# Performance work log

Measured on AMD Instinct MI355X. Metric: run time of the kernel, lower is better.

## Reference

```python
import jax, jax.numpy as jnp
import numpy as np

BETA = 0.25


def _l2_normalize(v, eps=1e-12):
    # matches torch F.normalize(dim=-1): v / max(||v||, eps)
    n = jnp.linalg.norm(v, axis=-1, keepdims=True)
    return v / jnp.maximum(n, eps)


def _cosine_sim(a, b, eps=1e-8):
    # matches torch F.cosine_similarity(dim=-1)
    na = jnp.maximum(jnp.linalg.norm(a, axis=-1), eps)
    nb = jnp.maximum(jnp.linalg.norm(b, axis=-1), eps)
    return jnp.sum(a * b, axis=-1) / (na * nb)


def setup_inputs() -> dict:
    key = jax.random.key(0)
    k1, k2 = jax.random.split(key)
    B, D, N = 32768, 256, 8192
    x = jax.random.normal(k1, (B, D), dtype=jnp.float32)
    # embedding init: uniform(-1/n_e, 1/n_e) as in the torch module
    embedding = jax.random.uniform(k2, (N, D), dtype=jnp.float32,
                                   minval=-1.0 / N, maxval=1.0 / N)
    return {"x": x, "embedding": embedding}


def reference(x, embedding):
    latent = x                                   # (B, D)
    codebook = embedding                         # (N, D)
    latent_norm = _l2_normalize(latent)
    codebook_norm = _l2_normalize(codebook)
    sim = jnp.einsum('bd,nd->bn', latent_norm, codebook_norm)  # (B, N)
    distances = 1.0 - sim
    indices = jnp.argmin(distances, axis=-1)     # (B,) int
    codebook_vec = codebook[indices]             # (B, D) gather
    dot = jnp.sum(latent * codebook_vec, axis=-1, keepdims=True)
    norm_sq = jnp.sum(codebook_vec * codebook_vec, axis=-1, keepdims=True)
    scalar = dot / (norm_sq + 1e-8)              # (B, 1)
    proj_vec = scalar * codebook_vec             # (B, D)
    # use_ema=True branch: only commitment loss (proj_vec detached)
    commit = _cosine_sim(jax.lax.stop_gradient(proj_vec), latent)
    loss = BETA * jnp.mean(1.0 - commit)
    # straight-through
    x_q = x + jax.lax.stop_gradient(proj_vec - x)
    return (x_q, loss, indices, scalar[:, 0])
```

## Files before the change

### kernel.cpp

```cpp
#include <hip/hip_runtime.h>
#include <hip/hip_bf16.h>
#include <hip/hip_fp16.h>
#include <cstdint>
#include <cstddef>

#define B_ROWS 32768
#define DIM    256
#define NBLK64 128
#define CERT_M 3.0e-3f
#define PRE_M  3.0e-3f

typedef _Float16 f16x8 __attribute__((ext_vector_type(8)));
typedef float    f32x4 __attribute__((ext_vector_type(4)));
typedef unsigned short u16x8 __attribute__((ext_vector_type(8)));

#define WS_XBF     ((size_t)0)
#define WS_CBBF    ((size_t)16777216)
#define WS_TOPINFO ((size_t)20971520)
#define WS_CNORM   ((size_t)54525952)
#define WS_LPART   ((size_t)54591488)

#define OUT_XQ   ((size_t)0)
#define OUT_LOSS ((size_t)8388608)
#define OUT_IDX  ((size_t)8388609)
#define OUT_SCAL ((size_t)(8388609 + 32768))

__device__ inline double wave_sum_d(double v){ for (int d = 1; d < 64; d <<= 1) v += __shfl_xor(v, d); return v; }
__device__ inline unsigned umax_(unsigned a, unsigned b){ return a > b ? a : b; }
__device__ inline unsigned umin_(unsigned a, unsigned b){ return a < b ? a : b; }

__device__ inline float kinvb(unsigned k){ return __uint_as_float(k & 0xFFFFE000u); }

__device__ inline void load16_lds(const void* g, void* l) {
    __builtin_amdgcn_global_load_lds(
        (const __attribute__((address_space(1))) unsigned int*)g,
        (__attribute__((address_space(3))) unsigned int*)l, 16, 0, 0);
}

__global__ __launch_bounds__(256)
void prep_kernel(const float* __restrict__ x, const float* __restrict__ cb,
                 ushort* __restrict__ xbf, ushort* __restrict__ cbbf,
                 double* __restrict__ inv_cnorm) {
    int gw   = blockIdx.x * 4 + (threadIdx.x >> 6);
    int lane = threadIdx.x & 63;
    bool is_cb = gw >= B_ROWS;
    int row  = is_cb ? gw - B_ROWS : gw;
    const float* src = is_cb ? cb + (size_t)row * DIM : x + (size_t)row * DIM;
    ushort*      dst = is_cb ? cbbf + (size_t)row * DIM : xbf + (size_t)row * DIM;

    float4 v = ((const float4*)src)[lane];
    double ss = (double)v.x * v.x + (double)v.y * v.y + (double)v.z * v.z + (double)v.w * v.w;
    ss = wave_sum_d(ss);
    float inv = 1.f / fmaxf(sqrtf((float)ss), 1e-12f);
    ushort4 o;
    o.x = __half_as_ushort(__float2half(v.x * inv));
    o.y = __half_as_ushort(__float2half(v.y * inv));
    o.z = __half_as_ushort(__float2half(v.z * inv));
    o.w = __half_as_ushort(__float2half(v.w * inv));
    ((ushort4*)dst)[lane] = o;
    if (is_cb && lane == 0) inv_cnorm[row] = 1.0 / sqrt(ss);
}

__global__ __launch_bounds__(512, 2)
void simmax_kernel(const ushort* __restrict__ xbf, const ushort* __restrict__ cbbf,
                   uint2* __restrict__ topinfo) {
    __shared__ __align__(16) ushort Cs[2][256 * 64];
    __shared__ __align__(16) ushort Xs[2][256 * 64];

    const int t    = threadIdx.x;
    const int xcd  = blockIdx.x & 7;
    const int lidx = blockIdx.x >> 3;
    const int bm   = xcd * 4 + (lidx & 3);
    const int bn   = lidx >> 2;
    const int cn0  = bm * 256;
    const int rm0  = bn * 256;

    const int wid  = t >> 6, lane = t & 63;
    const int wm   = wid >> 2;
    const int wn   = wid & 3;
    const int q    = lane >> 4, r16 = lane & 15;

    const int srow = t >> 3;
    const int cpos = t & 7;
    const int csrc = cpos ^ (srow & 7);
    const ushort* cbsrc = cbbf + (size_t)(cn0 + srow) * DIM + csrc * 8;
    const ushort* xsrc  = xbf  + (size_t)(rm0 + srow) * DIM + csrc * 8;
    const int ldst = srow * 64 + cpos * 8;

    const int g0  = q ^ (r16 & 7);
    const int g1  = g0 ^ 4;
    const int crb = (wm * 128 + r16) * 64;
    const int xrb = (wn * 64  + r16) * 64;

    f32x4 acc[8][4];
#pragma unroll
    for (int i = 0; i < 8; ++i)
#pragma unroll
        for (int j = 0; j < 4; ++j) acc[i][j] = (f32x4){2.f, 2.f, 2.f, 2.f};

    f16x8 cf[4][2], xf0[2][2], xf1[2][2];

#define SCHED0 __builtin_amdgcn_sched_barrier(0)
#define SBAR do { SCHED0; __builtin_amdgcn_s_barrier(); SCHED0; } while (0)
#define WLG0 do { asm volatile("s_waitcnt lgkmcnt(0)" ::: "memory"); SCHED0; } while (0)
#define WVM(N) do { asm volatile("s_waitcnt vmcnt(" #N ")" ::: "memory"); SCHED0; } while (0)

#define ST_C(B,KT,H) do { \
    load16_lds(cbsrc + ((H)*128     ) * DIM + (KT)*64, &Cs[B][ldst + ((H)*128     ) * 64]); \
    load16_lds(cbsrc + ((H)*128 + 64) * DIM + (KT)*64, &Cs[B][ldst + ((H)*128 + 64) * 64]); \
} while (0)
#define ST_X(B,KT,H) do { \
    load16_lds(xsrc  + ((H)*128     ) * DIM + (KT)*64, &Xs[B][ldst + ((H)*128     ) * 64]); \
    load16_lds(xsrc  + ((H)*128 + 64) * DIM + (KT)*64, &Xs[B][ldst + ((H)*128 + 64) * 64]); \
} while (0)

#define RD_C(HM,B) do { \
    _Pragma("unroll") \
    for (int m2_ = 0; m2_ < 4; ++m2_) { \
        const ushort* p_ = &Cs[B][crb + ((HM)*64 + m2_*16) * 64]; \
        cf[m2_][0] = *(const f16x8*)(p_ + g0 * 8); \
        cf[m2_][1] = *(const f16x8*)(p_ + g1 * 8); \
    } } while (0)
#define RD_X(DST,HN,B) do { \
    _Pragma("unroll") \
    for (int n2_ = 0; n2_ < 2; ++n2_) { \
        const ushort* p_ = &Xs[B][xrb + ((HN)*32 + n2_*16) * 64]; \
        DST[n2_][0] = *(const f16x8*)(p_ + g0 * 8); \
        DST[n2_][1] = *(const f16x8*)(p_ + g1 * 8); \
    } } while (0)

#define MMQ(HM,HN,XF) do { \
    __builtin_amdgcn_s_setprio(1); \
    _Pragma("unroll") \
    for (int m2_ = 0; m2_ < 4; ++m2_) \
    _Pragma("unroll") \
    for (int n2_ = 0; n2_ < 2; ++n2_) \
    _Pragma("unroll") \
    for (int kk_ = 0; kk_ < 2; ++kk_) \
        acc[(HM)*4 + m2_][(HN)*2 + n2_] = __builtin_amdgcn_mfma_f32_16x16x32_f16( \
            cf[m2_][kk_], XF[n2_][kk_], acc[(HM)*4 + m2_][(HN)*2 + n2_], 0, 0, 0); \
    __builtin_amdgcn_s_setprio(0); \
} while (0)

    ST_X(0,0,0); ST_X(0,0,1); ST_C(0,0,0); ST_C(0,0,1);
    ST_X(1,1,0);
    WVM(2); SBAR;

    RD_C(0,0); RD_X(xf0,0,0); ST_X(1,1,1); SBAR; WLG0; MMQ(0,0,xf0); SBAR;
    RD_X(xf1,1,0);            ST_C(1,1,0); SBAR; WLG0; MMQ(0,1,xf1); SBAR;
    RD_C(1,0);                ST_C(1,1,1); SBAR; WLG0; MMQ(1,1,xf1); SBAR;
    ST_X(0,2,0); WVM(2);                   SBAR;       MMQ(1,0,xf0); SBAR;
    RD_C(0,1); RD_X(xf0,0,1); ST_X(0,2,1); SBAR; WLG0; MMQ(0,0,xf0); SBAR;
    RD_X(xf1,1,1);            ST_C(0,2,0); SBAR; WLG0; MMQ(0,1,xf1); SBAR;
    RD_C(1,1);                ST_C(0,2,1); SBAR; WLG0; MMQ(1,1,xf1); SBAR;
    ST_X(1,3,0); WVM(2);                   SBAR;       MMQ(1,0,xf0); SBAR;
    RD_C(0,0); RD_X(xf0,0,0); ST_X(1,3,1); SBAR; WLG0; MMQ(0,0,xf0); SBAR;
    RD_X(xf1,1,0);            ST_C(1,3,0); SBAR; WLG0; MMQ(0,1,xf1); SBAR;
    RD_C(1,0);                ST_C(1,3,1); SBAR; WLG0; MMQ(1,1,xf1); SBAR;
    WVM(0);                                SBAR;       MMQ(1,0,xf0); SBAR;
    RD_C(0,1); RD_X(xf0,0,1);              SBAR; WLG0; MMQ(0,0,xf0); SBAR;
    RD_X(xf1,1,1);                         SBAR; WLG0; MMQ(0,1,xf1); SBAR;
    RD_C(1,1);                             SBAR; WLG0; MMQ(1,1,xf1); SBAR;
                                                       MMQ(1,0,xf0);

    const int cb0 = 8191 - (cn0 + wm * 128 + q * 4);
#pragma unroll
    for (int ni = 0; ni < 4; ++ni) {
        unsigned r1v[2], r2v[2];
#pragma unroll
        for (int b2 = 0; b2 < 2; ++b2) {
            const unsigned cbb = (unsigned)(cb0 - b2 * 64);
            unsigned k[16];
#pragma unroll
            for (int m2 = 0; m2 < 4; ++m2)
#pragma unroll
                for (int r = 0; r < 4; ++r)
                    k[m2 * 4 + r] = (__float_as_uint(acc[b2 * 4 + m2][ni][r]) & 0xFFFFE000u)
                                  | (cbb - (unsigned)(m2 * 16 + r));
            unsigned h0[8], l0[8];
#pragma unroll
            for (int i = 0; i < 8; ++i) { h0[i] = umax_(k[2*i], k[2*i+1]); l0[i] = umin_(k[2*i], k[2*i+1]); }
            unsigned h1[4], l1[4];
#pragma unroll
            for (int i = 0; i < 4; ++i) { h1[i] = umax_(h0[2*i], h0[2*i+1]); l1[i] = umin_(h0[2*i], h0[2*i+1]); }
            unsigned h2a = umax_(h1[0], h1[1]), l2a = umin_(h1[0], h1[1]);
            unsigned h2b = umax_(h1[2], h1[3]), l2b = umin_(h1[2], h1[3]);
            unsigned m1  = umax_(h2a, h2b);
            unsigned lt  = umin_(h2a, h2b);
            unsigned s0  = umax_(umax_(umax_(l0[0], l0[1]), umax_(l0[2], l0[3])),
                                 umax_(umax_(l0[4], l0[5]), umax_(l0[6], l0[7])));
            unsigned s1  = umax_(umax_(l1[0], l1[1]), umax_(l1[2], l1[3]));
            unsigned m2v = umax_(umax_(s0, s1), umax_(umax_(l2a, l2b), lt));
#pragma unroll
            for (int d = 16; d < 64; d <<= 1) {
                unsigned o1 = (unsigned)__shfl_xor((int)m1, d);
                unsigned o2 = (unsigned)__shfl_xor((int)m2v, d);
                unsigned lo = m1 < o1 ? m1 : o1;
                m2v = umax_(umax_(m2v, o2), lo);
                m1  = umax_(m1, o1);
            }
            r1v[b2] = m1; r2v[b2] = m2v;
        }
        if (q == 0) {
            const int rowg = rm0 + wn * 64 + ni * 16 + r16;
            uint4 o; o.x = r1v[0]; o.y = r2v[0]; o.z = r1v[1]; o.w = r2v[1];
            *(uint4*)(topinfo + (size_t)rowg * NBLK64 + bm * 4 + wm * 2) = o;
        }
    }
#undef SCHED0
#undef SBAR
#undef WLG0
#undef WVM
#undef ST_C
#undef ST_X
#undef RD_C
#undef RD_X
#undef MMQ
}

__global__ __launch_bounds__(256)
void argmax_kernel(const float* __restrict__ x, const float* __restrict__ cb,
                   const ushort* __restrict__ xbf, const ushort* __restrict__ cbbf,
                   const uint2* __restrict__ topinfo,
                   const double* __restrict__ inv_cnorm,
                   float* __restrict__ out, float* __restrict__ loss_part) {
    __shared__ float lsum[4];
    const int w    = threadIdx.x >> 6;
    const int row  = blockIdx.x * 4 + w;
    const int lane = threadIdx.x & 63;

    uint4 tt = ((const uint4*)(topinfo + (size_t)row * NBLK64))[lane];
    unsigned k1[2] = {tt.x, tt.z};
    unsigned k2[2] = {tt.y, tt.w};

    unsigned W = umax_(k1[0], k1[1]);
    for (int d = 1; d < 64; d <<= 1) W = umax_(W, (unsigned)__shfl_xor((int)W, d));
    unsigned R = umax_((k1[0] == W) ? k2[0] : k1[0], (k1[1] == W) ? k2[1] : k1[1]);
    for (int d = 1; d < 64; d <<= 1) R = umax_(R, (unsigned)__shfl_xor((int)R, d));

    float v1w = kinvb(W);
    float rvf = kinvb(R);

    float4 xv = ((const float4*)(x + (size_t)row * DIM))[lane];

    int best_i;
    if (v1w - rvf > CERT_M) {
        best_i = 8191 - (int)(W & 0x1FFFu);
    } else {
        const int c = lane >> 3, e = lane & 7;
        float xh[32];
#pragma unroll
        for (int k4 = 0; k4 < 4; ++k4) {
            u16x8 hx = ((const u16x8*)(xbf + (size_t)row * DIM + e * 32))[k4];
#pragma unroll
            for (int j = 0; j < 8; ++j)
                xh[k4 * 8 + j] = __half2float(__ushort_as_half((ushort)hx[j]));
        }

        double best_s = -1e300;
        int bi = 0x7fffffff;
        auto exact_eval = [&](int n) {
            float4 cv = ((const float4*)(cb + (size_t)n * DIM))[lane];
            double s = (double)xv.x * cv.x + (double)xv.y * cv.y +
                       (double)xv.z * cv.z + (double)xv.w * cv.w;
            s = wave_sum_d(s);
            s *= inv_cnorm[n];
            if (s > best_s || (s == best_s && n < bi)) { best_s = s; bi = n; }
        };

        const float thrblk = v1w - CERT_M;
        const float thrpre = v1w - 2.0f - PRE_M;
        float v1f[2] = {kinvb(k1[0]), kinvb(k1[1])};
#pragma unroll
        for (int s = 0; s < 2; ++s) {
            unsigned long long bm = __ballot(v1f[s] >= thrblk);
            while (bm) {
                int src = __ffsll((unsigned long long)bm) - 1;
                bm &= bm - 1;
                int blk = src * 2 + s;
#pragma unroll 1
                for (int sub = 0; sub < 8; ++sub) {
                    int n = blk * 64 + sub * 8 + c;
                    float s0 = 0.f, s1 = 0.f, s2 = 0.f, s3 = 0.f;
#pragma unroll
                    for (int k4 = 0; k4 < 4; ++k4) {
                        u16x8 chv = ((const u16x8*)(cbbf + (size_t)n * DIM + e * 32))[k4];
#pragma unroll
                        for (int j = 0; j < 8; ++j) {
                            float cf = __half2float(__ushort_as_half((ushort)chv[j]));
                            float xf = xh[k4 * 8 + j];
                            if ((j & 3) == 0) s0 = fmaf(xf, cf, s0);
                            else if ((j & 3) == 1) s1 = fmaf(xf, cf, s1);
                            else if ((j & 3) == 2) s2 = fmaf(xf, cf, s2);
                            else s3 = fmaf(xf, cf, s3);
                        }
                    }
                    float ps = (s0 + s1) + (s2 + s3);
                    ps += __shfl_xor(ps, 1);
                    ps += __shfl_xor(ps, 2);
                    ps += __shfl_xor(ps, 4);
                    unsigned long long sv = __ballot(e == 0 && ps >= thrpre);
                    while (sv) {
                        int b = __ffsll((unsigned long long)sv) - 1;
                        sv &= sv - 1;
                        exact_eval(blk * 64 + sub * 8 + (b >> 3));
                    }
                }
            }
        }
        for (int d = 1; d < 64; d <<= 1) {
            double os = __shfl_xor(best_s, d);
            int    oi = __shfl_xor(bi, d);
            if (os > best_s || (os == best_s && oi < bi)) { best_s = os; bi = oi; }
        }
        best_i = bi;
    }

    float4 cv = ((const float4*)(cb + (size_t)best_i * DIM))[lane];
    float dot = xv.x * cv.x + xv.y * cv.y + xv.z * cv.z + xv.w * cv.w;
    float nsq = cv.x * cv.x + cv.y * cv.y + cv.z * cv.z + cv.w * cv.w;
    float xsq = xv.x * xv.x + xv.y * xv.y + xv.z * xv.z + xv.w * xv.w;
    for (int d = 1; d < 64; d <<= 1) {
        dot += __shfl_xor(dot, d);
        nsq += __shfl_xor(nsq, d);
        xsq += __shfl_xor(xsq, d);
    }
    float scalar = dot / (nsq + 1e-8f);
    float4 pj = {scalar * cv.x, scalar * cv.y, scalar * cv.z, scalar * cv.w};
    ((float4*)(out + OUT_XQ + (size_t)row * DIM))[lane] = pj;

    float pn = fmaxf(sqrtf(scalar * scalar * nsq), 1e-8f);
    float xn = fmaxf(sqrtf(xsq), 1e-8f);
    float commit = (scalar * dot) / (pn * xn);
    if (lane == 0) {
        lsum[w] = 1.f - commit;
        out[OUT_IDX + row]  = (float)best_i;
        out[OUT_SCAL + row] = scalar;
    }
    __syncthreads();
    if (threadIdx.x == 0)
        loss_part[blockIdx.x] = lsum[0] + lsum[1] + lsum[2] + lsum[3];
}

__global__ __launch_bounds__(256)
void loss_kernel(const float* __restrict__ part, float* __restrict__ out) {
    __shared__ float ws_[4];
    float s = 0.f;
    for (int i = threadIdx.x; i < 8192; i += 256) s += part[i];
    for (int d = 1; d < 64; d <<= 1) s += __shfl_xor(s, d);
    if ((threadIdx.x & 63) == 0) ws_[threadIdx.x >> 6] = s;
    __syncthreads();
    if (threadIdx.x == 0)
        out[OUT_LOSS] = 0.25f * (ws_[0] + ws_[1] + ws_[2] + ws_[3]) * (1.0f / 32768.0f);
}

extern "C" void kernel_launch(void* const* d_in, const int* in_sizes, int n_in,
                              void* d_out, int out_size, void* d_ws, size_t ws_size,
                              hipStream_t stream) {
    const float* x  = (const float*)d_in[0];
    const float* cb = (const float*)d_in[1];
    float* out = (float*)d_out;
    char*  ws  = (char*)d_ws;
    ushort* xbf     = (ushort*)(ws + WS_XBF);
    ushort* cbbf    = (ushort*)(ws + WS_CBBF);
    uint2*  topinfo = (uint2*)(ws + WS_TOPINFO);
    double* inv_cn  = (double*)(ws + WS_CNORM);
    float*  loss_part = (float*)(ws + WS_LPART);

    hipLaunchKernelGGL(prep_kernel, dim3((B_ROWS + 8192) / 4), dim3(256), 0, stream,
                       x, cb, xbf, cbbf, inv_cn);
    hipLaunchKernelGGL(simmax_kernel, dim3((B_ROWS / 256) * (8192 / 256)), dim3(512), 0, stream,
                       xbf, cbbf, topinfo);
    hipLaunchKernelGGL(argmax_kernel, dim3(B_ROWS / 4), dim3(256), 0, stream,
                       x, cb, xbf, cbbf, topinfo, inv_cn, out, loss_part);
    hipLaunchKernelGGL(loss_kernel, dim3(1), dim3(256), 0, stream, loss_part, out);
}
```

Before: 334.3 us.

## Make simmax kernel persistent, looping over 16 row tiles with cross-tile prefetch

The similarity/top-2 kernel becomes persistent: 256 blocks each handle one codebook tile and iterate over 16 row tiles of x. Loads for the next tile's first K-slices are issued during the tail of the current tile, so launch/prologue cost is amortized and the pipeline stays full across tiles. The codebook tile stays in the same block, but the codebook tile is reloaded every iteration anyway; the risk is lower parallelism (256 blocks with 2 per CU may underfill 256 CUs) and a serial epilogue reduction that is now not overlapped with other blocks' MMA.

```diff
diff --git a/kernel.cpp b/kernel.cpp
--- a/kernel.cpp
+++ b/kernel.cpp
@@ -67,24 +67,22 @@
     __shared__ __align__(16) ushort Cs[2][256 * 64];
     __shared__ __align__(16) ushort Xs[2][256 * 64];
 
-    const int t    = threadIdx.x;
-    const int xcd  = blockIdx.x & 7;
-    const int lidx = blockIdx.x >> 3;
-    const int bm   = xcd * 4 + (lidx & 3);
-    const int bn   = lidx >> 2;
+    const int t512 = threadIdx.x;
+    const int b    = blockIdx.x;
+    const int bm   = (b & 7) * 4 + ((b >> 3) & 3);
+    const int bn0  = (b >> 5) * 16;
     const int cn0  = bm * 256;
-    const int rm0  = bn * 256;
-
-    const int wid  = t >> 6, lane = t & 63;
+
+    const int wid  = t512 >> 6, lane = t512 & 63;
     const int wm   = wid >> 2;
     const int wn   = wid & 3;
     const int q    = lane >> 4, r16 = lane & 15;
 
-    const int srow = t >> 3;
-    const int cpos = t & 7;
+    const int srow = t512 >> 3;
+    const int cpos = t512 & 7;
     const int csrc = cpos ^ (srow & 7);
-    const ushort* cbsrc = cbbf + (size_t)(cn0 + srow) * DIM + csrc * 8;
-    const ushort* xsrc  = xbf  + (size_t)(rm0 + srow) * DIM + csrc * 8;
+    const ushort* cbsrc  = cbbf + (size_t)(cn0 + srow) * DIM + csrc * 8;
+    const ushort* xfirst = xbf  + ((size_t)bn0 * 256 + srow) * DIM + csrc * 8;
     const int ldst = srow * 64 + cpos * 8;
 
     const int g0  = q ^ (r16 & 7);
@@ -93,11 +91,6 @@
     const int xrb = (wn * 64  + r16) * 64;
 
     f32x4 acc[8][4];
-#pragma unroll
-    for (int i = 0; i < 8; ++i)
-#pragma unroll
-        for (int j = 0; j < 4; ++j) acc[i][j] = (f32x4){2.f, 2.f, 2.f, 2.f};
-
     f16x8 cf[4][2], xf0[2][2], xf1[2][2];
 
 #define SCHED0 __builtin_amdgcn_sched_barrier(0)
@@ -109,9 +102,9 @@
     load16_lds(cbsrc + ((H)*128     ) * DIM + (KT)*64, &Cs[B][ldst + ((H)*128     ) * 64]); \
     load16_lds(cbsrc + ((H)*128 + 64) * DIM + (KT)*64, &Cs[B][ldst + ((H)*128 + 64) * 64]); \
 } while (0)
-#define ST_X(B,KT,H) do { \
-    load16_lds(xsrc  + ((H)*128     ) * DIM + (KT)*64, &Xs[B][ldst + ((H)*128     ) * 64]); \
-    load16_lds(xsrc  + ((H)*128 + 64) * DIM + (KT)*64, &Xs[B][ldst + ((H)*128 + 64) * 64]); \
+#define ST_X(B,KT,H,P) do { \
+    load16_lds((P)  + ((H)*128     ) * DIM + (KT)*64, &Xs[B][ldst + ((H)*128     ) * 64]); \
+    load16_lds((P)  + ((H)*128 + 64) * DIM + (KT)*64, &Xs[B][ldst + ((H)*128 + 64) * 64]); \
 } while (0)
 
 #define RD_C(HM,B) do { \
@@ -142,71 +135,93 @@
     __builtin_amdgcn_s_setprio(0); \
 } while (0)
 
-    ST_X(0,0,0); ST_X(0,0,1); ST_C(0,0,0); ST_C(0,0,1);
-    ST_X(1,1,0);
+#pragma unroll
+    for (int i = 0; i < 8; ++i)
+#pragma unroll
+        for (int j = 0; j < 4; ++j) acc[i][j] = (f32x4){2.f, 2.f, 2.f, 2.f};
+
+    const ushort* xA = xfirst;
+    ST_X(0,0,0,xA); ST_X(0,0,1,xA); ST_C(0,0,0); ST_C(0,0,1);
+    ST_X(1,1,0,xA);
     WVM(2); SBAR;
 
-    RD_C(0,0); RD_X(xf0,0,0); ST_X(1,1,1); SBAR; WLG0; MMQ(0,0,xf0); SBAR;
-    RD_X(xf1,1,0);            ST_C(1,1,0); SBAR; WLG0; MMQ(0,1,xf1); SBAR;
-    RD_C(1,0);                ST_C(1,1,1); SBAR; WLG0; MMQ(1,1,xf1); SBAR;
-    ST_X(0,2,0); WVM(2);                   SBAR;       MMQ(1,0,xf0); SBAR;
-    RD_C(0,1); RD_X(xf0,0,1); ST_X(0,2,1); SBAR; WLG0; MMQ(0,0,xf0); SBAR;
-    RD_X(xf1,1,1);            ST_C(0,2,0); SBAR; WLG0; MMQ(0,1,xf1); SBAR;
-    RD_C(1,1);                ST_C(0,2,1); SBAR; WLG0; MMQ(1,1,xf1); SBAR;
-    ST_X(1,3,0); WVM(2);                   SBAR;       MMQ(1,0,xf0); SBAR;
-    RD_C(0,0); RD_X(xf0,0,0); ST_X(1,3,1); SBAR; WLG0; MMQ(0,0,xf0); SBAR;
-    RD_X(xf1,1,0);            ST_C(1,3,0); SBAR; WLG0; MMQ(0,1,xf1); SBAR;
-    RD_C(1,0);                ST_C(1,3,1); SBAR; WLG0; MMQ(1,1,xf1); SBAR;
-    WVM(0);                                SBAR;       MMQ(1,0,xf0); SBAR;
-    RD_C(0,1); RD_X(xf0,0,1);              SBAR; WLG0; MMQ(0,0,xf0); SBAR;
-    RD_X(xf1,1,1);                         SBAR; WLG0; MMQ(0,1,xf1); SBAR;
-    RD_C(1,1);                             SBAR; WLG0; MMQ(1,1,xf1); SBAR;
-                                                       MMQ(1,0,xf0);
-
-    const int cb0 = 8191 - (cn0 + wm * 128 + q * 4);
-#pragma unroll
-    for (int ni = 0; ni < 4; ++ni) {
-        unsigned r1v[2], r2v[2];
-#pragma unroll
-        for (int b2 = 0; b2 < 2; ++b2) {
-            const unsigned cbb = (unsigned)(cb0 - b2 * 64);
-            unsigned k[16];
-#pragma unroll
-            for (int m2 = 0; m2 < 4; ++m2)
-#pragma unroll
-                for (int r = 0; r < 4; ++r)
-                    k[m2 * 4 + r] = (__float_as_uint(acc[b2 * 4 + m2][ni][r]) & 0xFFFFE000u)
-                                  | (cbb - (unsigned)(m2 * 16 + r));
-            unsigned h0[8], l0[8];
-#pragma unroll
-            for (int i = 0; i < 8; ++i) { h0[i] = umax_(k[2*i], k[2*i+1]); l0[i] = umin_(k[2*i], k[2*i+1]); }
-            unsigned h1[4], l1[4];
-#pragma unroll
-            for (int i = 0; i < 4; ++i) { h1[i] = umax_(h0[2*i], h0[2*i+1]); l1[i] = umin_(h0[2*i], h0[2*i+1]); }
-            unsigned h2a = umax_(h1[0], h1[1]), l2a = umin_(h1[0], h1[1]);
-            unsigned h2b = umax_(h1[2], h1[3]), l2b = umin_(h1[2], h1[3]);
-            unsigned m1  = umax_(h2a, h2b);
-            unsigned lt  = umin_(h2a, h2b);
-            unsigned s0  = umax_(umax_(umax_(l0[0], l0[1]), umax_(l0[2], l0[3])),
-                                 umax_(umax_(l0[4], l0[5]), umax_(l0[6], l0[7])));
-            unsigned s1  = umax_(umax_(l1[0], l1[1]), umax_(l1[2], l1[3]));
-            unsigned m2v = umax_(umax_(s0, s1), umax_(umax_(l2a, l2b), lt));
-#pragma unroll
-            for (int d = 16; d < 64; d <<= 1) {
-                unsigned o1 = (unsigned)__shfl_xor((int)m1, d);
-                unsigned o2 = (unsigned)__shfl_xor((int)m2v, d);
-                unsigned lo = m1 < o1 ? m1 : o1;
-                m2v = umax_(umax_(m2v, o2), lo);
-                m1  = umax_(m1, o1);
+#pragma unroll 1
+    for (int t = 0; t < 16; ++t) {
+        const ushort* xB = (t == 15) ? xfirst : (xA + 256 * DIM);
+
+        RD_C(0,0); RD_X(xf0,0,0); ST_X(1,1,1,xA); SBAR; WLG0; MMQ(0,0,xf0); SBAR;
+        RD_X(xf1,1,0);            ST_C(1,1,0);    SBAR; WLG0; MMQ(0,1,xf1); SBAR;
+        RD_C(1,0);                ST_C(1,1,1);    SBAR; WLG0; MMQ(1,1,xf1); SBAR;
+        ST_X(0,2,0,xA); WVM(2);                   SBAR;       MMQ(1,0,xf0); SBAR;
+        RD_C(0,1); RD_X(xf0,0,1); ST_X(0,2,1,xA); SBAR; WLG0; MMQ(0,0,xf0); SBAR;
+        RD_X(xf1,1,1);            ST_C(0,2,0);    SBAR; WLG0; MMQ(0,1,xf1); SBAR;
+        RD_C(1,1);                ST_C(0,2,1);    SBAR; WLG0; MMQ(1,1,xf1); SBAR;
+        ST_X(1,3,0,xA); WVM(2);                   SBAR;       MMQ(1,0,xf0); SBAR;
+        RD_C(0,0); RD_X(xf0,0,0); ST_X(1,3,1,xA); SBAR; WLG0; MMQ(0,0,xf0); SBAR;
+        RD_X(xf1,1,0);            ST_C(1,3,0);    SBAR; WLG0; MMQ(0,1,xf1); SBAR;
+        RD_C(1,0);                ST_C(1,3,1);    SBAR; WLG0; MMQ(1,1,xf1); SBAR;
+        ST_X(0,0,0,xB); WVM(2);                   SBAR;       MMQ(1,0,xf0); SBAR;
+        RD_C(0,1); RD_X(xf0,0,1); ST_X(0,0,1,xB); SBAR; WLG0; MMQ(0,0,xf0); SBAR;
+        RD_X(xf1,1,1);            ST_C(0,0,0);    SBAR; WLG0; MMQ(0,1,xf1); SBAR;
+        RD_C(1,1);                ST_C(0,0,1);    SBAR; WLG0; MMQ(1,1,xf1); SBAR;
+        ST_X(1,1,0,xB); WVM(2);                   SBAR;       MMQ(1,0,xf0); SBAR;
+
+        const int rm0 = (bn0 + t) * 256;
+        const int cb0 = 8191 - (cn0 + wm * 128 + q * 4);
+#pragma unroll
+        for (int ni = 0; ni < 4; ++ni) {
+            unsigned r1v[2], r2v[2];
+#pragma unroll
+            for (int b2 = 0; b2 < 2; ++b2) {
+                const unsigned cbb = (unsigned)(cb0 - b2 * 64);
+                unsigned k[16];
+#pragma unroll
+                for (int m2 = 0; m2 < 4; ++m2)
+#pragma unroll
+                    for (int r = 0; r < 4; ++r)
+                        k[m2 * 4 + r] = (__float_as_uint(acc[b2 * 4 + m2][ni][r]) & 0xFFFFE000u)
+                                      | (cbb - (unsigned)(m2 * 16 + r));
+                unsigned h0[8], l0[8];
+#pragma unroll
+                for (int i = 0; i < 8; ++i) { h0[i] = umax_(k[2*i], k[2*i+1]); l0[i] = umin_(k[2*i], k[2*i+1]); }
+                unsigned h1[4], l1[4];
+#pragma unroll
+                for (int i = 0; i < 4; ++i) { h1[i] = umax_(h0[2*i], h0[2*i+1]); l1[i] = umin_(h0[2*i], h0[2*i+1]); }
+                unsigned h2a = umax_(h1[0], h1[1]), l2a = umin_(h1[0], h1[1]);
+                unsigned h2b = umax_(h1[2], h1[3]), l2b = umin_(h1[2], h1[3]);
+                unsigned m1  = umax_(h2a, h2b);
+                unsigned lt  = umin_(h2a, h2b);
+                unsigned s0  = umax_(umax_(umax_(l0[0], l0[1]), umax_(l0[2], l0[3])),
+                                     umax_(umax_(l0[4], l0[5]), umax_(l0[6], l0[7])));
+                unsigned s1  = umax_(umax_(l1[0], l1[1]), umax_(l1[2], l1[3]));
+                unsigned m2v = umax_(umax_(s0, s1), umax_(umax_(l2a, l2b), lt));
+#pragma unroll
+                for (int d = 16; d < 64; d <<= 1) {
+                    unsigned o1 = (unsigned)__shfl_xor((int)m1, d);
+                    unsigned o2 = (unsigned)__shfl_xor((int)m2v, d);
+                    unsigned lo = m1 < o1 ? m1 : o1;
+                    m2v = umax_(umax_(m2v, o2), lo);
+                    m1  = umax_(m1, o1);
+                }
+                r1v[b2] = m1; r2v[b2] = m2v;
             }
-            r1v[b2] = m1; r2v[b2] = m2v;
+            if (q == 0) {
+                const int rowg = rm0 + wn * 64 + ni * 16 + r16;
+                uint4 o; o.x = r1v[0]; o.y = r2v[0]; o.z = r1v[1]; o.w = r2v[1];
+                *(uint4*)(topinfo + (size_t)rowg * NBLK64 + bm * 4 + wm * 2) = o;
+            }
         }
-        if (q == 0) {
-            const int rowg = rm0 + wn * 64 + ni * 16 + r16;
-            uint4 o; o.x = r1v[0]; o.y = r2v[0]; o.z = r1v[1]; o.w = r2v[1];
-            *(uint4*)(topinfo + (size_t)rowg * NBLK64 + bm * 4 + wm * 2) = o;
-        }
+
+#pragma unroll
+        for (int i = 0; i < 8; ++i)
+#pragma unroll
+            for (int j = 0; j < 4; ++j) acc[i][j] = (f32x4){2.f, 2.f, 2.f, 2.f};
+
+        xA = xB;
     }
+
+    WVM(0);
+
 #undef SCHED0
 #undef SBAR
 #undef WLG0
@@ -369,7 +384,7 @@
 
     hipLaunchKernelGGL(prep_kernel, dim3((B_ROWS + 8192) / 4), dim3(256), 0, stream,
                        x, cb, xbf, cbbf, inv_cn);
-    hipLaunchKernelGGL(simmax_kernel, dim3((B_ROWS / 256) * (8192 / 256)), dim3(512), 0, stream,
+    hipLaunchKernelGGL(simmax_kernel, dim3(256), dim3(512), 0, stream,
                        xbf, cbbf, topinfo);
     hipLaunchKernelGGL(argmax_kernel, dim3(B_ROWS / 4), dim3(256), 0, stream,
                        x, cb, xbf, cbbf, topinfo, inv_cn, out, loss_part);
```

Result: slower. 428.2 us (+28.1%).

## Restructure simmax K-loop with triple-buffered X tiles and fewer barriers

Applied to the files above, without the earlier changes.

Rewrites the simmax GEMM main loop as a 4-step K loop. X tiles are triple-buffered and codebook fragments are double-buffered in registers (cfA/cfB), so LDS reads for the next half overlap MFMAs. Per-quarter barriers and explicit lgkmcnt waits are dropped in favour of one or two barriers per K step. The top-2 reduction for the first codebook half is interleaved with the last MFMAs to hide its latency. In exchange, LDS use rises from 128 KB to 160 KB per block, which may conflict with the 2-blocks-per-CU launch bound, and register pressure grows.

```diff
diff --git a/kernel.cpp b/kernel.cpp
--- a/kernel.cpp
+++ b/kernel.cpp
@@ -65,7 +65,7 @@
 void simmax_kernel(const ushort* __restrict__ xbf, const ushort* __restrict__ cbbf,
                    uint2* __restrict__ topinfo) {
     __shared__ __align__(16) ushort Cs[2][256 * 64];
-    __shared__ __align__(16) ushort Xs[2][256 * 64];
+    __shared__ __align__(16) ushort Xs[3][256 * 64];
 
     const int t    = threadIdx.x;
     const int xcd  = blockIdx.x & 7;
@@ -89,8 +89,6 @@
 
     const int g0  = q ^ (r16 & 7);
     const int g1  = g0 ^ 4;
-    const int crb = (wm * 128 + r16) * 64;
-    const int xrb = (wn * 64  + r16) * 64;
 
     f32x4 acc[8][4];
 #pragma unroll
@@ -98,38 +96,35 @@
 #pragma unroll
         for (int j = 0; j < 4; ++j) acc[i][j] = (f32x4){2.f, 2.f, 2.f, 2.f};
 
-    f16x8 cf[4][2], xf0[2][2], xf1[2][2];
+    f16x8 cfA[4][2], cfB[4][2], xp[2][2], xq[2][2];
 
 #define SCHED0 __builtin_amdgcn_sched_barrier(0)
-#define SBAR do { SCHED0; __builtin_amdgcn_s_barrier(); SCHED0; } while (0)
-#define WLG0 do { asm volatile("s_waitcnt lgkmcnt(0)" ::: "memory"); SCHED0; } while (0)
+#define SBAR do { __builtin_amdgcn_s_barrier(); SCHED0; } while (0)
 #define WVM(N) do { asm volatile("s_waitcnt vmcnt(" #N ")" ::: "memory"); SCHED0; } while (0)
 
-#define ST_C(B,KT,H) do { \
-    load16_lds(cbsrc + ((H)*128     ) * DIM + (KT)*64, &Cs[B][ldst + ((H)*128     ) * 64]); \
-    load16_lds(cbsrc + ((H)*128 + 64) * DIM + (KT)*64, &Cs[B][ldst + ((H)*128 + 64) * 64]); \
+#define ST4(DST, SRC, KT) do { \
+    load16_lds((SRC) + (size_t)  0 * DIM + (KT)*64, &(DST)[ldst +   0 * 64]); \
+    load16_lds((SRC) + (size_t) 64 * DIM + (KT)*64, &(DST)[ldst +  64 * 64]); \
+    load16_lds((SRC) + (size_t)128 * DIM + (KT)*64, &(DST)[ldst + 128 * 64]); \
+    load16_lds((SRC) + (size_t)192 * DIM + (KT)*64, &(DST)[ldst + 192 * 64]); \
 } while (0)
-#define ST_X(B,KT,H) do { \
-    load16_lds(xsrc  + ((H)*128     ) * DIM + (KT)*64, &Xs[B][ldst + ((H)*128     ) * 64]); \
-    load16_lds(xsrc  + ((H)*128 + 64) * DIM + (KT)*64, &Xs[B][ldst + ((H)*128 + 64) * 64]); \
-} while (0)
-
-#define RD_C(HM,B) do { \
+
+#define RD_C8(DST, BUF, HOFF) do { \
     _Pragma("unroll") \
     for (int m2_ = 0; m2_ < 4; ++m2_) { \
-        const ushort* p_ = &Cs[B][crb + ((HM)*64 + m2_*16) * 64]; \
-        cf[m2_][0] = *(const f16x8*)(p_ + g0 * 8); \
-        cf[m2_][1] = *(const f16x8*)(p_ + g1 * 8); \
+        const ushort* p_ = &(BUF)[(wm * 128 + (HOFF) + m2_ * 16 + r16) * 64]; \
+        DST[m2_][0] = *(const f16x8*)(p_ + g0 * 8); \
+        DST[m2_][1] = *(const f16x8*)(p_ + g1 * 8); \
     } } while (0)
-#define RD_X(DST,HN,B) do { \
+#define RD_X4(DST, BUF, HOFF) do { \
     _Pragma("unroll") \
     for (int n2_ = 0; n2_ < 2; ++n2_) { \
-        const ushort* p_ = &Xs[B][xrb + ((HN)*32 + n2_*16) * 64]; \
+        const ushort* p_ = &(BUF)[(wn * 64 + (HOFF) + n2_ * 16 + r16) * 64]; \
         DST[n2_][0] = *(const f16x8*)(p_ + g0 * 8); \
         DST[n2_][1] = *(const f16x8*)(p_ + g1 * 8); \
     } } while (0)
 
-#define MMQ(HM,HN,XF) do { \
+#define MMQ(CF, XF, HM, HN) do { \
     __builtin_amdgcn_s_setprio(1); \
     _Pragma("unroll") \
     for (int m2_ = 0; m2_ < 4; ++m2_) \
@@ -138,84 +133,96 @@
     _Pragma("unroll") \
     for (int kk_ = 0; kk_ < 2; ++kk_) \
         acc[(HM)*4 + m2_][(HN)*2 + n2_] = __builtin_amdgcn_mfma_f32_16x16x32_f16( \
-            cf[m2_][kk_], XF[n2_][kk_], acc[(HM)*4 + m2_][(HN)*2 + n2_], 0, 0, 0); \
+            CF[m2_][kk_], XF[n2_][kk_], acc[(HM)*4 + m2_][(HN)*2 + n2_], 0, 0, 0); \
     __builtin_amdgcn_s_setprio(0); \
 } while (0)
 
-    ST_X(0,0,0); ST_X(0,0,1); ST_C(0,0,0); ST_C(0,0,1);
-    ST_X(1,1,0);
-    WVM(2); SBAR;
-
-    RD_C(0,0); RD_X(xf0,0,0); ST_X(1,1,1); SBAR; WLG0; MMQ(0,0,xf0); SBAR;
-    RD_X(xf1,1,0);            ST_C(1,1,0); SBAR; WLG0; MMQ(0,1,xf1); SBAR;
-    RD_C(1,0);                ST_C(1,1,1); SBAR; WLG0; MMQ(1,1,xf1); SBAR;
-    ST_X(0,2,0); WVM(2);                   SBAR;       MMQ(1,0,xf0); SBAR;
-    RD_C(0,1); RD_X(xf0,0,1); ST_X(0,2,1); SBAR; WLG0; MMQ(0,0,xf0); SBAR;
-    RD_X(xf1,1,1);            ST_C(0,2,0); SBAR; WLG0; MMQ(0,1,xf1); SBAR;
-    RD_C(1,1);                ST_C(0,2,1); SBAR; WLG0; MMQ(1,1,xf1); SBAR;
-    ST_X(1,3,0); WVM(2);                   SBAR;       MMQ(1,0,xf0); SBAR;
-    RD_C(0,0); RD_X(xf0,0,0); ST_X(1,3,1); SBAR; WLG0; MMQ(0,0,xf0); SBAR;
-    RD_X(xf1,1,0);            ST_C(1,3,0); SBAR; WLG0; MMQ(0,1,xf1); SBAR;
-    RD_C(1,0);                ST_C(1,3,1); SBAR; WLG0; MMQ(1,1,xf1); SBAR;
-    WVM(0);                                SBAR;       MMQ(1,0,xf0); SBAR;
-    RD_C(0,1); RD_X(xf0,0,1);              SBAR; WLG0; MMQ(0,0,xf0); SBAR;
-    RD_X(xf1,1,1);                         SBAR; WLG0; MMQ(0,1,xf1); SBAR;
-    RD_C(1,1);                             SBAR; WLG0; MMQ(1,1,xf1); SBAR;
-                                                       MMQ(1,0,xf0);
+#define TOP2(B2, NI, M1O, M2O) do { \
+    const unsigned cbb_ = (unsigned)(cb0 - (B2) * 64); \
+    unsigned k_[16]; \
+    _Pragma("unroll") \
+    for (int m2_ = 0; m2_ < 4; ++m2_) \
+    _Pragma("unroll") \
+    for (int r_ = 0; r_ < 4; ++r_) \
+        k_[m2_*4+r_] = (__float_as_uint(acc[(B2)*4 + m2_][NI][r_]) & 0xFFFFE000u) \
+                     | (cbb_ - (unsigned)(m2_*16 + r_)); \
+    unsigned h0_[8], l0_[8]; \
+    _Pragma("unroll") \
+    for (int i_ = 0; i_ < 8; ++i_) { h0_[i_] = umax_(k_[2*i_], k_[2*i_+1]); l0_[i_] = umin_(k_[2*i_], k_[2*i_+1]); } \
+    unsigned h1_[4], l1_[4]; \
+    _Pragma("unroll") \
+    for (int i_ = 0; i_ < 4; ++i_) { h1_[i_] = umax_(h0_[2*i_], h0_[2*i_+1]); l1_[i_] = umin_(h0_[2*i_], h0_[2*i_+1]); } \
+    unsigned h2a_ = umax_(h1_[0], h1_[1]), l2a_ = umin_(h1_[0], h1_[1]); \
+    unsigned h2b_ = umax_(h1_[2], h1_[3]), l2b_ = umin_(h1_[2], h1_[3]); \
+    unsigned m1_  = umax_(h2a_, h2b_); \
+    unsigned lt_  = umin_(h2a_, h2b_); \
+    unsigned s0_  = umax_(umax_(umax_(l0_[0], l0_[1]), umax_(l0_[2], l0_[3])), \
+                          umax_(umax_(l0_[4], l0_[5]), umax_(l0_[6], l0_[7]))); \
+    unsigned s1_  = umax_(umax_(l1_[0], l1_[1]), umax_(l1_[2], l1_[3])); \
+    unsigned m2v_ = umax_(umax_(s0_, s1_), umax_(umax_(l2a_, l2b_), lt_)); \
+    _Pragma("unroll") \
+    for (int d_ = 16; d_ < 64; d_ <<= 1) { \
+        unsigned o1_ = (unsigned)__shfl_xor((int)m1_, d_); \
+        unsigned o2_ = (unsigned)__shfl_xor((int)m2v_, d_); \
+        unsigned lo_ = m1_ < o1_ ? m1_ : o1_; \
+        m2v_ = umax_(umax_(m2v_, o2_), lo_); \
+        m1_  = umax_(m1_, o1_); \
+    } \
+    M1O = m1_; M2O = m2v_; \
+} while (0)
+
+    ST4(Cs[0], cbsrc, 0);
+    ST4(Xs[0], xsrc , 0);
+    ST4(Xs[1], xsrc , 1);
+    WVM(4);
+    SBAR;
+    RD_C8(cfA, Cs[0], 0);
 
     const int cb0 = 8191 - (cn0 + wm * 128 + q * 4);
+    unsigned r1a[4], r2a[4];
+
+#pragma unroll
+    for (int kt = 0; kt < 4; ++kt) {
+        const int cur = kt & 1, nxt = cur ^ 1;
+        if (kt < 3) ST4(Cs[nxt], cbsrc, kt + 1);
+        RD_X4(xp, Xs[kt % 3], 0);
+        RD_X4(xq, Xs[kt % 3], 32);
+        RD_C8(cfB, Cs[cur], 64);
+        MMQ(cfA, xp, 0, 0);
+        if (kt < 2) ST4(Xs[(kt + 2) % 3], xsrc, kt + 2);
+        MMQ(cfA, xq, 0, 1);
+        if (kt == 3) {
+#pragma unroll
+            for (int ni = 0; ni < 4; ++ni) TOP2(0, ni, r1a[ni], r2a[ni]);
+        }
+        if (kt < 3) {
+            if (kt < 2) { WVM(4); } else { WVM(0); }
+            SBAR;
+            RD_C8(cfA, Cs[nxt], 0);
+        }
+        MMQ(cfB, xq, 1, 1);
+        MMQ(cfB, xp, 1, 0);
+        if (kt < 3) SBAR;
+    }
+
 #pragma unroll
     for (int ni = 0; ni < 4; ++ni) {
-        unsigned r1v[2], r2v[2];
-#pragma unroll
-        for (int b2 = 0; b2 < 2; ++b2) {
-            const unsigned cbb = (unsigned)(cb0 - b2 * 64);
-            unsigned k[16];
-#pragma unroll
-            for (int m2 = 0; m2 < 4; ++m2)
-#pragma unroll
-                for (int r = 0; r < 4; ++r)
-                    k[m2 * 4 + r] = (__float_as_uint(acc[b2 * 4 + m2][ni][r]) & 0xFFFFE000u)
-                                  | (cbb - (unsigned)(m2 * 16 + r));
-            unsigned h0[8], l0[8];
-#pragma unroll
-            for (int i = 0; i < 8; ++i) { h0[i] = umax_(k[2*i], k[2*i+1]); l0[i] = umin_(k[2*i], k[2*i+1]); }
-            unsigned h1[4], l1[4];
-#pragma unroll
-            for (int i = 0; i < 4; ++i) { h1[i] = umax_(h0[2*i], h0[2*i+1]); l1[i] = umin_(h0[2*i], h0[2*i+1]); }
-            unsigned h2a = umax_(h1[0], h1[1]), l2a = umin_(h1[0], h1[1]);
-            unsigned h2b = umax_(h1[2], h1[3]), l2b = umin_(h1[2], h1[3]);
-            unsigned m1  = umax_(h2a, h2b);
-            unsigned lt  = umin_(h2a, h2b);
-            unsigned s0  = umax_(umax_(umax_(l0[0], l0[1]), umax_(l0[2], l0[3])),
-                                 umax_(umax_(l0[4], l0[5]), umax_(l0[6], l0[7])));
-            unsigned s1  = umax_(umax_(l1[0], l1[1]), umax_(l1[2], l1[3]));
-            unsigned m2v = umax_(umax_(s0, s1), umax_(umax_(l2a, l2b), lt));
-#pragma unroll
-            for (int d = 16; d < 64; d <<= 1) {
-                unsigned o1 = (unsigned)__shfl_xor((int)m1, d);
-                unsigned o2 = (unsigned)__shfl_xor((int)m2v, d);
-                unsigned lo = m1 < o1 ? m1 : o1;
-                m2v = umax_(umax_(m2v, o2), lo);
-                m1  = umax_(m1, o1);
-            }
-            r1v[b2] = m1; r2v[b2] = m2v;
-        }
+        unsigned r1b, r2b;
+        TOP2(1, ni, r1b, r2b);
         if (q == 0) {
             const int rowg = rm0 + wn * 64 + ni * 16 + r16;
-            uint4 o; o.x = r1v[0]; o.y = r2v[0]; o.z = r1v[1]; o.w = r2v[1];
+            uint4 o; o.x = r1a[ni]; o.y = r2a[ni]; o.z = r1b; o.w = r2b;
             *(uint4*)(topinfo + (size_t)rowg * NBLK64 + bm * 4 + wm * 2) = o;
         }
     }
 #undef SCHED0
 #undef SBAR
-#undef WLG0
 #undef WVM
-#undef ST_C
-#undef ST_X
-#undef RD_C
-#undef RD_X
+#undef ST4
+#undef RD_C8
+#undef RD_X4
 #undef MMQ
+#undef TOP2
 }
 
 __global__ __launch_bounds__(256)
```

Result: no change. 334.9 us (+0.2%).

## Evaluate lone block winners exactly and skip fp16 rescans when unneeded

Applied to the files above, without the earlier changes.

In the uncertain-row path, a block whose second-best key is below the threshold now has only its top candidate evaluated exactly in fp64, and the 64-entry fp16 block rescan runs only for blocks whose runner-up is also within margin. The fp16 row load moves inside that rescan branch. The accumulator bias drops from 2.0 to 1.25, presumably to give the packed key more precision, and the certification margin widens to match. Loss partials are now written per row and summed with float4 loads, which removes the block-level __syncthreads in argmax.

```diff
diff --git a/kernel.cpp b/kernel.cpp
--- a/kernel.cpp
+++ b/kernel.cpp
@@ -7,8 +7,9 @@
 #define B_ROWS 32768
 #define DIM    256
 #define NBLK64 128
-#define CERT_M 3.0e-3f
+#define CERT_M 4.5e-3f
 #define PRE_M  3.0e-3f
+#define KBIAS  1.25f
 
 typedef _Float16 f16x8 __attribute__((ext_vector_type(8)));
 typedef float    f32x4 __attribute__((ext_vector_type(4)));
@@ -18,7 +19,7 @@
 #define WS_CBBF    ((size_t)16777216)
 #define WS_TOPINFO ((size_t)20971520)
 #define WS_CNORM   ((size_t)54525952)
-#define WS_LPART   ((size_t)54591488)
+#define WS_LROW    ((size_t)54591488)
 
 #define OUT_XQ   ((size_t)0)
 #define OUT_LOSS ((size_t)8388608)
@@ -96,7 +97,7 @@
 #pragma unroll
     for (int i = 0; i < 8; ++i)
 #pragma unroll
-        for (int j = 0; j < 4; ++j) acc[i][j] = (f32x4){2.f, 2.f, 2.f, 2.f};
+        for (int j = 0; j < 4; ++j) acc[i][j] = (f32x4){KBIAS, KBIAS, KBIAS, KBIAS};
 
     f16x8 cf[4][2], xf0[2][2], xf1[2][2];
 
@@ -223,8 +224,7 @@
                    const ushort* __restrict__ xbf, const ushort* __restrict__ cbbf,
                    const uint2* __restrict__ topinfo,
                    const double* __restrict__ inv_cnorm,
-                   float* __restrict__ out, float* __restrict__ loss_part) {
-    __shared__ float lsum[4];
+                   float* __restrict__ out, float* __restrict__ loss_row) {
     const int w    = threadIdx.x >> 6;
     const int row  = blockIdx.x * 4 + w;
     const int lane = threadIdx.x & 63;
@@ -247,16 +247,6 @@
     if (v1w - rvf > CERT_M) {
         best_i = 8191 - (int)(W & 0x1FFFu);
     } else {
-        const int c = lane >> 3, e = lane & 7;
-        float xh[32];
-#pragma unroll
-        for (int k4 = 0; k4 < 4; ++k4) {
-            u16x8 hx = ((const u16x8*)(xbf + (size_t)row * DIM + e * 32))[k4];
-#pragma unroll
-            for (int j = 0; j < 8; ++j)
-                xh[k4 * 8 + j] = __half2float(__ushort_as_half((ushort)hx[j]));
-        }
-
         double best_s = -1e300;
         int bi = 0x7fffffff;
         auto exact_eval = [&](int n) {
@@ -269,41 +259,73 @@
         };
 
         const float thrblk = v1w - CERT_M;
-        const float thrpre = v1w - 2.0f - PRE_M;
-        float v1f[2] = {kinvb(k1[0]), kinvb(k1[1])};
+        const float thrpre = v1w - KBIAS - PRE_M;
+
+        unsigned long long evals[2], scans[2];
 #pragma unroll
         for (int s = 0; s < 2; ++s) {
-            unsigned long long bm = __ballot(v1f[s] >= thrblk);
-            while (bm) {
-                int src = __ffsll((unsigned long long)bm) - 1;
-                bm &= bm - 1;
-                int blk = src * 2 + s;
+            float v1f = kinvb(k1[s]);
+            float v2f = kinvb(k2[s]);
+            bool p2 = v2f >= thrblk;
+            evals[s] = __ballot((v1f >= thrblk) && !p2);
+            scans[s] = __ballot(p2);
+        }
+
+#pragma unroll
+        for (int s = 0; s < 2; ++s) {
+            unsigned long long bmv = evals[s];
+            while (bmv) {
+                int src = __ffsll(bmv) - 1;
+                bmv &= bmv - 1;
+                int kk = __shfl((int)k1[s], src);
+                exact_eval(8191 - (kk & 0x1FFF));
+            }
+        }
+
+        if (scans[0] | scans[1]) {
+            const int c = lane >> 3, e = lane & 7;
+            float xh[32];
+#pragma unroll
+            for (int k4 = 0; k4 < 4; ++k4) {
+                u16x8 hx = ((const u16x8*)(xbf + (size_t)row * DIM + e * 32))[k4];
+#pragma unroll
+                for (int j = 0; j < 8; ++j)
+                    xh[k4 * 8 + j] = __half2float(__ushort_as_half((ushort)hx[j]));
+            }
+#pragma unroll
+            for (int s = 0; s < 2; ++s) {
+                unsigned long long bmv = scans[s];
+                while (bmv) {
+                    int src = __ffsll(bmv) - 1;
+                    bmv &= bmv - 1;
+                    int blk = src * 2 + s;
 #pragma unroll 1
-                for (int sub = 0; sub < 8; ++sub) {
-                    int n = blk * 64 + sub * 8 + c;
-                    float s0 = 0.f, s1 = 0.f, s2 = 0.f, s3 = 0.f;
-#pragma unroll
-                    for (int k4 = 0; k4 < 4; ++k4) {
-                        u16x8 chv = ((const u16x8*)(cbbf + (size_t)n * DIM + e * 32))[k4];
-#pragma unroll
-                        for (int j = 0; j < 8; ++j) {
-                            float cf = __half2float(__ushort_as_half((ushort)chv[j]));
-                            float xf = xh[k4 * 8 + j];
-                            if ((j & 3) == 0) s0 = fmaf(xf, cf, s0);
-                            else if ((j & 3) == 1) s1 = fmaf(xf, cf, s1);
-                            else if ((j & 3) == 2) s2 = fmaf(xf, cf, s2);
-                            else s3 = fmaf(xf, cf, s3);
+                    for (int sub = 0; sub < 8; ++sub) {
+                        int n = blk * 64 + sub * 8 + c;
+                        float s0 = 0.f, s1 = 0.f, s2 = 0.f, s3 = 0.f;
+#pragma unroll
+                        for (int k4 = 0; k4 < 4; ++k4) {
+                            u16x8 chv = ((const u16x8*)(cbbf + (size_t)n * DIM + e * 32))[k4];
+#pragma unroll
+                            for (int j = 0; j < 8; ++j) {
+                                float cf = __half2float(__ushort_as_half((ushort)chv[j]));
+                                float xf = xh[k4 * 8 + j];
+                                if ((j & 3) == 0) s0 = fmaf(xf, cf, s0);
+                                else if ((j & 3) == 1) s1 = fmaf(xf, cf, s1);
+                                else if ((j & 3) == 2) s2 = fmaf(xf, cf, s2);
+                                else s3 = fmaf(xf, cf, s3);
+                            }
                         }
-                    }
-                    float ps = (s0 + s1) + (s2 + s3);
-                    ps += __shfl_xor(ps, 1);
-                    ps += __shfl_xor(ps, 2);
-                    ps += __shfl_xor(ps, 4);
-                    unsigned long long sv = __ballot(e == 0 && ps >= thrpre);
-                    while (sv) {
-                        int b = __ffsll((unsigned long long)sv) - 1;
-                        sv &= sv - 1;
-                        exact_eval(blk * 64 + sub * 8 + (b >> 3));
+                        float ps = (s0 + s1) + (s2 + s3);
+                        ps += __shfl_xor(ps, 1);
+                        ps += __shfl_xor(ps, 2);
+                        ps += __shfl_xor(ps, 4);
+                        unsigned long long sv = __ballot(e == 0 && ps >= thrpre);
+                        while (sv) {
+                            int b = __ffsll(sv) - 1;
+                            sv &= sv - 1;
+                            exact_eval(blk * 64 + sub * 8 + (b >> 3));
+                        }
                     }
                 }
             }
@@ -333,20 +355,21 @@
     float xn = fmaxf(sqrtf(xsq), 1e-8f);
     float commit = (scalar * dot) / (pn * xn);
     if (lane == 0) {
-        lsum[w] = 1.f - commit;
+        loss_row[row] = 1.f - commit;
         out[OUT_IDX + row]  = (float)best_i;
         out[OUT_SCAL + row] = scalar;
     }
-    __syncthreads();
-    if (threadIdx.x == 0)
-        loss_part[blockIdx.x] = lsum[0] + lsum[1] + lsum[2] + lsum[3];
 }
 
 __global__ __launch_bounds__(256)
 void loss_kernel(const float* __restrict__ part, float* __restrict__ out) {
     __shared__ float ws_[4];
+    const float4* p4 = (const float4*)part;
     float s = 0.f;
-    for (int i = threadIdx.x; i < 8192; i += 256) s += part[i];
+    for (int i = threadIdx.x; i < 8192; i += 256) {
+        float4 v = p4[i];
+        s += (v.x + v.y) + (v.z + v.w);
+    }
     for (int d = 1; d < 64; d <<= 1) s += __shfl_xor(s, d);
     if ((threadIdx.x & 63) == 0) ws_[threadIdx.x >> 6] = s;
     __syncthreads();
@@ -365,13 +388,13 @@
     ushort* cbbf    = (ushort*)(ws + WS_CBBF);
     uint2*  topinfo = (uint2*)(ws + WS_TOPINFO);
     double* inv_cn  = (double*)(ws + WS_CNORM);
-    float*  loss_part = (float*)(ws + WS_LPART);
+    float*  loss_row = (float*)(ws + WS_LROW);
 
     hipLaunchKernelGGL(prep_kernel, dim3((B_ROWS + 8192) / 4), dim3(256), 0, stream,
                        x, cb, xbf, cbbf, inv_cn);
     hipLaunchKernelGGL(simmax_kernel, dim3((B_ROWS / 256) * (8192 / 256)), dim3(512), 0, stream,
                        xbf, cbbf, topinfo);
     hipLaunchKernelGGL(argmax_kernel, dim3(B_ROWS / 4), dim3(256), 0, stream,
-                       x, cb, xbf, cbbf, topinfo, inv_cn, out, loss_part);
-    hipLaunchKernelGGL(loss_kernel, dim3(1), dim3(256), 0, stream, loss_part, out);
-}
+                       x, cb, xbf, cbbf, topinfo, inv_cn, out, loss_row);
+    hipLaunchKernelGGL(loss_kernel, dim3(1), dim3(256), 0, stream, loss_row, out);
+}
```

New measurement: 287.5 us. 14.0% less time.
